# Kernel tuning notes

Measured on AMD Instinct MI355X. Metric: run time of the kernel, lower is better.

Reference implementation:

```python
import jax, jax.numpy as jnp
import numpy as np

N = 50000      # nodes
E = 800000     # edges (avg degree 16)
G = 128        # g_dim (input feature dim)
H1 = 128       # h1_dim (RGCN output dim)
H2 = 32        # h2_dim (per-head channels)
HEADS = 4
R = 6          # num_relations
OUT = H2 * HEADS  # 128, BatchNorm width
BN_EPS = 1e-5


def setup_inputs() -> dict:
    key = jax.random.key(0)
    k = jax.random.split(key, 16)
    s = 0.05
    return {
        "node_features": jax.random.normal(k[0], (N, G), jnp.float32),
        "node_type": jax.random.randint(k[1], (N,), 0, 3),
        "edge_index": jax.random.randint(k[2], (2, E), 0, N),
        "edge_type": jax.random.randint(k[3], (E,), 0, R),
        # RGCNConv params (root_weight=True, bias=True, aggr='mean')
        "W_rel": jax.random.normal(k[4], (R, G, H1), jnp.float32) * s,
        "W_root": jax.random.normal(k[5], (G, H1), jnp.float32) * s,
        "b_rgcn": jnp.zeros((H1,), jnp.float32),
        # TransformerConv params (concat=True, root_weight=True via lin_skip)
        "Wq": jax.random.normal(k[6], (H1, OUT), jnp.float32) * s,
        "bq": jnp.zeros((OUT,), jnp.float32),
        "Wk": jax.random.normal(k[7], (H1, OUT), jnp.float32) * s,
        "bk": jnp.zeros((OUT,), jnp.float32),
        "Wv": jax.random.normal(k[8], (H1, OUT), jnp.float32) * s,
        "bv": jnp.zeros((OUT,), jnp.float32),
        "Wskip": jax.random.normal(k[9], (H1, OUT), jnp.float32) * s,
        "bskip": jnp.zeros((OUT,), jnp.float32),
        # BatchNorm1d affine params
        "bn_gamma": jnp.ones((OUT,), jnp.float32),
        "bn_beta": jnp.zeros((OUT,), jnp.float32),
    }


def _gnn_forward(node_features, edge_index, edge_type,
                 W_rel, W_root, b_rgcn,
                 Wq, bq, Wk, bk, Wv, bv, Wskip, bskip,
                 bn_gamma, bn_beta):
    src, dst = edge_index[0], edge_index[1]  # message flows src (j) -> dst (i)

    # ---- RGCNConv with mean aggregation per relation ----
    # Transform all nodes under every relation: [R, N, H1]
    xt = jnp.einsum('nd,rdo->rno', node_features, W_rel)
    msg = xt[edge_type, src]                          # [E, H1]
    seg = edge_type * N + dst                         # composite (relation, dst) segment id
    agg = jax.ops.segment_sum(msg, seg, num_segments=R * N).reshape(R, N, H1)
    cnt = jax.ops.segment_sum(jnp.ones((E,), msg.dtype), seg,
                              num_segments=R * N).reshape(R, N)
    x = node_features @ W_root + b_rgcn + (agg / jnp.maximum(cnt, 1.0)[:, :, None]).sum(0)

    # ---- TransformerConv (heads=HEADS, concat=True) ----
    q = (x @ Wq + bq).reshape(N, HEADS, H2)
    kk = (x @ Wk + bk).reshape(N, HEADS, H2)
    v = (x @ Wv + bv).reshape(N, HEADS, H2)

    score = (q[dst] * kk[src]).sum(-1) / np.sqrt(H2)  # [E, HEADS]
    m = jax.ops.segment_max(score, dst, num_segments=N)   # -inf for isolated nodes
    m = jnp.where(jnp.isfinite(m), m, 0.0)
    ex = jnp.exp(score - m[dst])
    den = jax.ops.segment_sum(ex, dst, num_segments=N)
    alpha = ex / (den[dst] + 1e-16)                   # [E, HEADS]

    out = jax.ops.segment_sum(alpha[:, :, None] * v[src], dst,
                              num_segments=N).reshape(N, OUT)
    out = out + x @ Wskip + bskip                     # skip / root connection

    # ---- BatchNorm1d (training-mode batch stats) + LeakyReLU(0.01) ----
    mu = out.mean(0)
    var = out.var(0)  # biased, as torch uses for normalization
    y = (out - mu) * jax.lax.rsqrt(var + BN_EPS) * bn_gamma + bn_beta
    return jax.nn.leaky_relu(y, negative_slope=0.01)


def reference(node_features, node_type, edge_index, edge_type,
              W_rel, W_root, b_rgcn,
              Wq, bq, Wk, bk, Wv, bv, Wskip, bskip,
              bn_gamma, bn_beta):
    # node_type is accepted but unused, matching the original forward.
    return _gnn_forward(node_features, edge_index, edge_type,
                        W_rel, W_root, b_rgcn,
                        Wq, bq, Wk, bk, Wv, bv, Wskip, bskip,
                        bn_gamma, bn_beta)
```

## Files before the change

### kernel.cpp

```cpp
#include <hip/hip_runtime.h>
#include <hip/hip_fp16.h>
#include <stdint.h>

#define G      128
#define OUTW   128
#define RNUM   6

typedef unsigned short us;
typedef _Float16 f16x8 __attribute__((ext_vector_type(8)));
typedef float    f32x4 __attribute__((ext_vector_type(4)));

__device__ inline float h2f(us u) { __half h; *(us*)&h = u; return __half2float(h); }
__device__ inline us f2h(float f) { __half h = __float2half(f); return *(us*)&h; }
__device__ inline float2 h22(int u) { return __half22float2(*(__half2*)&u); }

union FragU { f16x8 v; ushort4 u[2]; };

__global__ void count_kernel(const int* __restrict__ ei, const int* __restrict__ et,
                             int* __restrict__ segcnt, int N, int E) {
    int e = blockIdx.x * blockDim.x + threadIdx.x;
    if (e >= E) return;
    int dst = ei[E + e];
    int r   = et[e];
    atomicAdd(&segcnt[dst * RNUM + r], 1);
}

__global__ __launch_bounds__(256)
void scan_part(const int* __restrict__ cnt, int* __restrict__ bsum, int n) {
    __shared__ int s[256];
    int base = blockIdx.x * 1024, t = threadIdx.x;
    int v = 0;
    for (int j = 0; j < 4; ++j) { int idx = base + j * 256 + t; if (idx < n) v += cnt[idx]; }
    s[t] = v; __syncthreads();
    for (int off = 128; off; off >>= 1) { if (t < off) s[t] += s[t + off]; __syncthreads(); }
    if (!t) bsum[blockIdx.x] = s[0];
}

__global__ __launch_bounds__(512)
void scan_top(const int* __restrict__ bsum, int* __restrict__ boff,
              int* __restrict__ segptr, int nb, int n) {
    __shared__ int s[512];
    int t = threadIdx.x;
    int v = (t < nb) ? bsum[t] : 0;
    s[t] = v;
    __syncthreads();
    for (int off = 1; off < 512; off <<= 1) {
        int y = (t >= off) ? s[t - off] : 0;
        __syncthreads();
        s[t] += y;
        __syncthreads();
    }
    if (t < nb) boff[t + 1] = s[t];
    if (!t) boff[0] = 0;
    if (t == nb - 1) segptr[n] = s[t];
}

__global__ __launch_bounds__(256)
void scan_apply(const int* __restrict__ cnt, const int* __restrict__ boff,
                int* __restrict__ segptr, int* __restrict__ cursor, int n) {
    __shared__ int L[1024];
    __shared__ int SS[256];
    int base = blockIdx.x * 1024, t = threadIdx.x;
    for (int j = 0; j < 4; ++j) { int idx = base + j * 256 + t; L[j * 256 + t] = (idx < n) ? cnt[idx] : 0; }
    __syncthreads();
    int s0 = L[t*4] + L[t*4+1] + L[t*4+2] + L[t*4+3];
    SS[t] = s0; __syncthreads();
    for (int off = 1; off < 256; off <<= 1) {
        int y = (t >= off) ? SS[t - off] : 0;
        __syncthreads();
        SS[t] += y;
        __syncthreads();
    }
    int e0 = (t ? SS[t - 1] : 0) + boff[blockIdx.x];
    int4 ov;
    int a;
    a = L[t*4+0]; ov.x = e0; e0 += a;
    a = L[t*4+1]; ov.y = e0; e0 += a;
    a = L[t*4+2]; ov.z = e0; e0 += a;
    a = L[t*4+3]; ov.w = e0; e0 += a;
    int idx0 = base + t * 4;
    if (idx0 + 3 < n) {
        *(int4*)(segptr + idx0) = ov;
        *(int4*)(cursor + idx0) = ov;
    } else {
        int vals[4] = {ov.x, ov.y, ov.z, ov.w};
        for (int k = 0; k < 4; ++k)
            if (idx0 + k < n) { segptr[idx0 + k] = vals[k]; cursor[idx0 + k] = vals[k]; }
    }
}

__global__ void scatter_kernel(const int* __restrict__ ei, const int* __restrict__ et,
                               int* __restrict__ cursor, unsigned* __restrict__ esrc,
                               int N, int E) {
    int e = blockIdx.x * blockDim.x + threadIdx.x;
    if (e >= E) return;
    int src = ei[e];
    int dst = ei[E + e];
    int r   = et[e];
    int pos = atomicAdd(&cursor[dst * RNUM + r], 1);
    esrc[pos] = (unsigned)src;
}

__global__ __launch_bounds__(256)
void prep_kernel(const float* __restrict__ x, us* __restrict__ xh,
                 const float* __restrict__ Wrel, const float* __restrict__ Wroot,
                 ushort4* __restrict__ Btr,
                 const float* __restrict__ Wq, const float* __restrict__ Wk,
                 const float* __restrict__ Wv, const float* __restrict__ Ws,
                 ushort4* __restrict__ Btq, int xblocks) {
    int b = blockIdx.x;
    if (b < xblocks) {
        int i = b * 256 + threadIdx.x;
        float4 a = ((const float4*)x)[2*i];
        float4 c = ((const float4*)x)[2*i+1];
        ushort4 u0 = { f2h(a.x), f2h(a.y), f2h(a.z), f2h(a.w) };
        ushort4 u1 = { f2h(c.x), f2h(c.y), f2h(c.z), f2h(c.w) };
        ((ushort4*)xh)[2*i]   = u0;
        ((ushort4*)xh)[2*i+1] = u1;
    } else if (b < xblocks + 112) {
        int idx = (b - xblocks) * 256 + threadIdx.x;
        int kq = idx >> 7, n = idx & 127;
        ushort4 o;
        us* op = (us*)&o;
#pragma unroll
        for (int i = 0; i < 4; ++i) {
            int k = 4 * kq + i;
            float v = (k < 768) ? Wrel[(size_t)k * 128 + n] : Wroot[(size_t)(k - 768) * 128 + n];
            op[i] = f2h(v);
        }
        Btr[idx] = o;
    } else {
        int idx = (b - xblocks - 112) * 256 + threadIdx.x;
        int kq = idx >> 9, n = idx & 511;
        int quad = n >> 7, nl = n & 127;
        const float* W = (quad == 0) ? Wq : (quad == 1) ? Wk : (quad == 2) ? Wv : Ws;
        ushort4 o;
        us* op = (us*)&o;
#pragma unroll
        for (int i = 0; i < 4; ++i) {
            int k = 4 * kq + i;
            op[i] = f2h(W[(size_t)k * 128 + nl]);
        }
        Btq[idx] = o;
    }
}

__global__ __launch_bounds__(256)
void agg_kernel(const us* __restrict__ xh, const int* __restrict__ segptr,
                const unsigned* __restrict__ esrc, us* __restrict__ meanh, int N) {
    const int wv = threadIdx.x >> 6, l = threadIdx.x & 63;
    const int i = blockIdx.x * 4 + wv;
    if (i >= N) return;
    const int e0 = __builtin_amdgcn_readfirstlane(segptr[i * RNUM]);
    const int e1 = __builtin_amdgcn_readfirstlane(segptr[i * RNUM + RNUM]);

    int rcur = 0;
    int sstart = e0;
    int bnext = __builtin_amdgcn_readfirstlane(segptr[i * RNUM + 1]);
    float2 a = {0.f, 0.f};
    us* wbase = meanh + (size_t)i * 768 + 2 * l;

#define FLUSH() { \
    float sc_ = 1.f / fmaxf((float)(bnext - sstart), 1.f); \
    ushort2 t2_ = { f2h(a.x * sc_), f2h(a.y * sc_) }; \
    *(ushort2*)(wbase + rcur * 128) = t2_; \
    a.x = 0.f; a.y = 0.f; \
    sstart = bnext; ++rcur; \
    if (rcur < RNUM) bnext = __builtin_amdgcn_readfirstlane(segptr[i * RNUM + rcur + 1]); }

#define GET(J) ((unsigned)__shfl((int)pv, (J)))
#define LX(Q)  (*(const ushort2*)(xh + (size_t)(Q) * G + 2 * l))
#define STEP(U) { while (p >= bnext && rcur < RNUM - 1) FLUSH(); \
                  a.x += h2f((U).x); a.y += h2f((U).y); ++p; }

    int p = e0;
    for (int wb = e0; wb < e1; wb += 64) {
        const int nc = min(64, e1 - wb);
        unsigned pv = (wb + l < e1) ? esrc[wb + l] : 0u;
        int j = 0;
        while (j + 8 <= nc) {
            unsigned q0 = GET(j+0), q1 = GET(j+1), q2 = GET(j+2), q3 = GET(j+3);
            unsigned q4 = GET(j+4), q5 = GET(j+5), q6 = GET(j+6), q7 = GET(j+7);
            ushort2 u0 = LX(q0), u1 = LX(q1), u2 = LX(q2), u3 = LX(q3);
            ushort2 u4 = LX(q4), u5 = LX(q5), u6 = LX(q6), u7 = LX(q7);
            STEP(u0); STEP(u1); STEP(u2); STEP(u3);
            STEP(u4); STEP(u5); STEP(u6); STEP(u7);
            j += 8;
        }
        while (j + 2 <= nc) {
            unsigned q0 = GET(j), q1 = GET(j+1);
            ushort2 u0 = LX(q0), u1 = LX(q1);
            STEP(u0); STEP(u1);
            j += 2;
        }
        if (j < nc) {
            unsigned q0 = GET(j);
            ushort2 u0 = LX(q0);
            STEP(u0);
            ++j;
        }
    }
    while (rcur < RNUM) FLUSH();
#undef STEP
#undef LX
#undef GET
#undef FLUSH
}

__global__ __launch_bounds__(256)
void rgcn_mfma4(const us* __restrict__ xh, const us* __restrict__ meanh,
                const ushort4* __restrict__ Btr, const float* __restrict__ brg,
                us* __restrict__ xrh, int N) {
    const int tid = threadIdx.x;
    const int w = tid >> 6, l = tid & 63;
    const int lh = l >> 4, lm = l & 15;
    const int rowbase = blockIdx.x * 128 + w * 32;

    const us* am[2];
    const us* ar[2];
#pragma unroll
    for (int tt = 0; tt < 2; ++tt) {
        int gr = min(rowbase + tt * 16 + lm, N - 1);
        am[tt] = meanh + (size_t)gr * 768;
        ar[tt] = xh + (size_t)gr * 128;
    }

    f32x4 acc[2][8];
#pragma unroll
    for (int tt = 0; tt < 2; ++tt)
#pragma unroll
        for (int ct = 0; ct < 8; ++ct) {
            float b = brg[ct * 16 + lm];
            acc[tt][ct] = (f32x4){b, b, b, b};
        }

    for (int s = 0; s < 24; ++s) {
        const int kqg = s * 8 + lh;
        const ushort4* B0 = Btr + (size_t)kqg * 128 + lm;
        const ushort4* B1 = B0 + 4 * 128;
        FragU bf[8];
#pragma unroll
        for (int ct = 0; ct < 8; ++ct) { bf[ct].u[0] = B0[ct * 16]; bf[ct].u[1] = B1[ct * 16]; }
#pragma unroll
        for (int tt = 0; tt < 2; ++tt) {
            FragU af;
            af.u[0] = *(const ushort4*)(am[tt] + s * 32 + 4 * lh);
            af.u[1] = *(const ushort4*)(am[tt] + s * 32 + 4 * lh + 16);
#pragma unroll
            for (int ct = 0; ct < 8; ++ct)
                acc[tt][ct] = __builtin_amdgcn_mfma_f32_16x16x32_f16(af.v, bf[ct].v, acc[tt][ct], 0, 0, 0);
        }
    }
#pragma unroll
    for (int s = 0; s < 4; ++s) {
        const int kqg = 192 + s * 8 + lh;
        const ushort4* B0 = Btr + (size_t)kqg * 128 + lm;
        const ushort4* B1 = B0 + 4 * 128;
        FragU bf[8];
#pragma unroll
        for (int ct = 0; ct < 8; ++ct) { bf[ct].u[0] = B0[ct * 16]; bf[ct].u[1] = B1[ct * 16]; }
#pragma unroll
        for (int tt = 0; tt < 2; ++tt) {
            FragU af;
            af.u[0] = *(const ushort4*)(ar[tt] + s * 32 + 4 * lh);
            af.u[1] = *(const ushort4*)(ar[tt] + s * 32 + 4 * lh + 16);
#pragma unroll
            for (int ct = 0; ct < 8; ++ct)
                acc[tt][ct] = __builtin_amdgcn_mfma_f32_16x16x32_f16(af.v, bf[ct].v, acc[tt][ct], 0, 0, 0);
        }
    }

#pragma unroll
    for (int tt = 0; tt < 2; ++tt)
#pragma unroll
        for (int ct = 0; ct < 8; ++ct)
#pragma unroll
            for (int i = 0; i < 4; ++i) {
                int r = rowbase + tt * 16 + 4 * lh + i;
                if (r < N) xrh[(size_t)r * 128 + ct * 16 + lm] = f2h(acc[tt][ct][i]);
            }
}

__global__ __launch_bounds__(256)
void qkvs_mfma3(const us* __restrict__ xrh, const ushort4* __restrict__ Btq,
                const float* __restrict__ bq, const float* __restrict__ bk,
                const float* __restrict__ bv, const float* __restrict__ bs,
                us* __restrict__ qsh, us* __restrict__ kvh, int N) {
    const int tid = threadIdx.x;
    const int quad = tid >> 6, l = tid & 63;
    const int lh = l >> 4, lm = l & 15;
    const int base = blockIdx.x * 32;
    const float* bias = (quad == 0) ? bq : (quad == 1) ? bk : (quad == 2) ? bv : bs;

    const us* ap[2];
#pragma unroll
    for (int tt = 0; tt < 2; ++tt) {
        int ar = min(base + tt * 16 + lm, N - 1);
        ap[tt] = xrh + (size_t)ar * 128;
    }

    f32x4 acc[2][8];
#pragma unroll
    for (int tt = 0; tt < 2; ++tt)
#pragma unroll
        for (int ct = 0; ct < 8; ++ct) {
            float b = bias[ct * 16 + lm];
            acc[tt][ct] = (f32x4){b, b, b, b};
        }

#pragma unroll
    for (int s = 0; s < 4; ++s) {
        const int kq = s * 8 + lh;
        const ushort4* B0 = Btq + (size_t)kq * 512 + quad * 128 + lm;
        const ushort4* B1 = B0 + 4 * 512;
        FragU bf[8];
#pragma unroll
        for (int ct = 0; ct < 8; ++ct) { bf[ct].u[0] = B0[ct * 16]; bf[ct].u[1] = B1[ct * 16]; }
#pragma unroll
        for (int tt = 0; tt < 2; ++tt) {
            FragU af;
            af.u[0] = *(const ushort4*)(ap[tt] + kq * 4);
            af.u[1] = *(const ushort4*)(ap[tt] + kq * 4 + 16);
#pragma unroll
            for (int ct = 0; ct < 8; ++ct)
                acc[tt][ct] = __builtin_amdgcn_mfma_f32_16x16x32_f16(af.v, bf[ct].v, acc[tt][ct], 0, 0, 0);
        }
    }

    if (quad == 0 || quad == 3) {
        const int off = (quad == 0) ? 0 : 128;
#pragma unroll
        for (int tt = 0; tt < 2; ++tt)
#pragma unroll
            for (int ct = 0; ct < 8; ++ct)
#pragma unroll
                for (int i = 0; i < 4; ++i) {
                    int r = base + tt * 16 + 4 * lh + i;
                    if (r < N) qsh[(size_t)r * 256 + off + ct * 16 + lm] = f2h(acc[tt][ct][i]);
                }
    } else {
        const int off = (quad == 1) ? 0 : 2;
#pragma unroll
        for (int tt = 0; tt < 2; ++tt)
#pragma unroll
            for (int ct = 0; ct < 8; ++ct)
#pragma unroll
                for (int i = 0; i < 4; ++i) {
                    int r = base + tt * 16 + 4 * lh + i;
                    int col = ct * 16 + lm;
                    if (r < N) kvh[(size_t)r * 256 + (col >> 1) * 4 + (col & 1) + off] = f2h(acc[tt][ct][i]);
                }
    }
}

__global__ __launch_bounds__(256)
void attn_kernel(const us* __restrict__ qsh, const us* __restrict__ kvh,
                 const int* __restrict__ segptr, const unsigned* __restrict__ esrc,
                 float* __restrict__ out, float* __restrict__ bnS,
                 float* __restrict__ bnQ, int N) {
    __shared__ float sS[128], sQ[128];
    const int tid = threadIdx.x;
    if (tid < 128) { sS[tid] = 0.f; sQ[tid] = 0.f; }
    __syncthreads();

    const int wv = tid >> 6, l = tid & 63;
    const int hh = l >> 5, ll = l & 31;
    const int stride = gridDim.x * 8;
    const float QS = 0.17677669529663687f;
    float4 bsum = {0,0,0,0}, bsq = {0,0,0,0};

#define SCORE(D, S) { \
    float2 ka_ = h22((D).x), kb_ = h22((D).z); \
    float t_ = q4.x*ka_.x + q4.y*ka_.y + q4.z*kb_.x + q4.w*kb_.y; \
    t_ += __shfl_xor(t_, 1, 8); t_ += __shfl_xor(t_, 2, 8); t_ += __shfl_xor(t_, 4, 8); \
    S = t_; }

    for (int ibase = blockIdx.x * 8 + wv * 2; ibase < N; ibase += stride) {
        const bool act = (ibase + hh) < N;
        const int i = min(ibase + hh, N - 1);

        int2 qu = *(const int2*)(qsh + (size_t)i * 256 + 4 * ll);
        float2 qa = h22(qu.x), qb = h22(qu.y);
        float4 q4 = { qa.x * QS, qa.y * QS, qb.x * QS, qb.y * QS };

        float m = -INFINITY, den = 0.f;
        float4 acc = {0,0,0,0};
        const int e0 = segptr[(size_t)i * RNUM], e1 = segptr[(size_t)i * RNUM + RNUM];

        for (int wb = e0; wb < e1; wb += 32) {
            const int nc = min(32, e1 - wb);
            unsigned pv = (wb + ll < e1) ? esrc[wb + ll] : 0u;
            int j = 0;
            for (; j + 8 <= nc; j += 8) {
                unsigned p0 = (unsigned)__shfl((int)pv, j+0, 32);
                unsigned p1 = (unsigned)__shfl((int)pv, j+1, 32);
                unsigned p2 = (unsigned)__shfl((int)pv, j+2, 32);
                unsigned p3 = (unsigned)__shfl((int)pv, j+3, 32);
                unsigned p4 = (unsigned)__shfl((int)pv, j+4, 32);
                unsigned p5 = (unsigned)__shfl((int)pv, j+5, 32);
                unsigned p6 = (unsigned)__shfl((int)pv, j+6, 32);
                unsigned p7 = (unsigned)__shfl((int)pv, j+7, 32);
                int4 d0 = *(const int4*)(kvh + (size_t)p0 * 256 + 8 * ll);
                int4 d1 = *(const int4*)(kvh + (size_t)p1 * 256 + 8 * ll);
                int4 d2 = *(const int4*)(kvh + (size_t)p2 * 256 + 8 * ll);
                int4 d3 = *(const int4*)(kvh + (size_t)p3 * 256 + 8 * ll);
                int4 d4 = *(const int4*)(kvh + (size_t)p4 * 256 + 8 * ll);
                int4 d5 = *(const int4*)(kvh + (size_t)p5 * 256 + 8 * ll);
                int4 d6 = *(const int4*)(kvh + (size_t)p6 * 256 + 8 * ll);
                int4 d7 = *(const int4*)(kvh + (size_t)p7 * 256 + 8 * ll);
                float s0, s1, s2, s3, s4, s5, s6, s7;
                SCORE(d0, s0); SCORE(d1, s1); SCORE(d2, s2); SCORE(d3, s3);
                SCORE(d4, s4); SCORE(d5, s5); SCORE(d6, s6); SCORE(d7, s7);
                float mx = fmaxf(m, fmaxf(
                    fmaxf(fmaxf(s0, s1), fmaxf(s2, s3)),
                    fmaxf(fmaxf(s4, s5), fmaxf(s6, s7))));
                float rs = __expf(m - mx);
                float w0 = __expf(s0 - mx), w1 = __expf(s1 - mx);
                float w2 = __expf(s2 - mx), w3 = __expf(s3 - mx);
                float w4 = __expf(s4 - mx), w5 = __expf(s5 - mx);
                float w6 = __expf(s6 - mx), w7 = __expf(s7 - mx);
                den = den * rs + (((w0 + w1) + (w2 + w3)) + ((w4 + w5) + (w6 + w7)));
                float2 va0 = h22(d0.y), vb0 = h22(d0.w);
                float2 va1 = h22(d1.y), vb1 = h22(d1.w);
                float2 va2 = h22(d2.y), vb2 = h22(d2.w);
                float2 va3 = h22(d3.y), vb3 = h22(d3.w);
                float2 va4 = h22(d4.y), vb4 = h22(d4.w);
                float2 va5 = h22(d5.y), vb5 = h22(d5.w);
                float2 va6 = h22(d6.y), vb6 = h22(d6.w);
                float2 va7 = h22(d7.y), vb7 = h22(d7.w);
                acc.x = acc.x * rs + ((w0*va0.x + w1*va1.x) + (w2*va2.x + w3*va3.x))
                                   + ((w4*va4.x + w5*va5.x) + (w6*va6.x + w7*va7.x));
                acc.y = acc.y * rs + ((w0*va0.y + w1*va1.y) + (w2*va2.y + w3*va3.y))
                                   + ((w4*va4.y + w5*va5.y) + (w6*va6.y + w7*va7.y));
                acc.z = acc.z * rs + ((w0*vb0.x + w1*vb1.x) + (w2*vb2.x + w3*vb3.x))
                                   + ((w4*vb4.x + w5*vb5.x) + (w6*vb6.x + w7*vb7.x));
                acc.w = acc.w * rs + ((w0*vb0.y + w1*vb1.y) + (w2*vb2.y + w3*vb3.y))
                                   + ((w4*vb4.y + w5*vb5.y) + (w6*vb6.y + w7*vb7.y));
                m = mx;
            }
            for (; j + 4 <= nc; j += 4) {
                unsigned p0 = (unsigned)__shfl((int)pv, j+0, 32);
                unsigned p1 = (unsigned)__shfl((int)pv, j+1, 32);
                unsigned p2 = (unsigned)__shfl((int)pv, j+2, 32);
                unsigned p3 = (unsigned)__shfl((int)pv, j+3, 32);
                int4 d0 = *(const int4*)(kvh + (size_t)p0 * 256 + 8 * ll);
                int4 d1 = *(const int4*)(kvh + (size_t)p1 * 256 + 8 * ll);
                int4 d2 = *(const int4*)(kvh + (size_t)p2 * 256 + 8 * ll);
                int4 d3 = *(const int4*)(kvh + (size_t)p3 * 256 + 8 * ll);
                float s0, s1, s2, s3;
                SCORE(d0, s0); SCORE(d1, s1); SCORE(d2, s2); SCORE(d3, s3);
                float mx = fmaxf(m, fmaxf(fmaxf(s0, s1), fmaxf(s2, s3)));
                float rs = __expf(m - mx);
                float w0 = __expf(s0 - mx), w1 = __expf(s1 - mx);
                float w2 = __expf(s2 - mx), w3 = __expf(s3 - mx);
                den = den * rs + ((w0 + w1) + (w2 + w3));
                float2 va0 = h22(d0.y), vb0 = h22(d0.w);
                float2 va1 = h22(d1.y), vb1 = h22(d1.w);
                float2 va2 = h22(d2.y), vb2 = h22(d2.w);
                float2 va3 = h22(d3.y), vb3 = h22(d3.w);
                acc.x = acc.x * rs + w0*va0.x + w1*va1.x + w2*va2.x + w3*va3.x;
                acc.y = acc.y * rs + w0*va0.y + w1*va1.y + w2*va2.y + w3*va3.y;
                acc.z = acc.z * rs + w0*vb0.x + w1*vb1.x + w2*vb2.x + w3*vb3.x;
                acc.w = acc.w * rs + w0*vb0.y + w1*vb1.y + w2*vb2.y + w3*vb3.y;
                m = mx;
            }
            for (; j < nc; ++j) {
                unsigned p0 = (unsigned)__shfl((int)pv, j, 32);
                int4 d0 = *(const int4*)(kvh + (size_t)p0 * 256 + 8 * ll);
                float s0; SCORE(d0, s0);
                float mx = fmaxf(m, s0);
                float rs = __expf(m - mx);
                float w0 = __expf(s0 - mx);
                den = den * rs + w0;
                float2 va0 = h22(d0.y), vb0 = h22(d0.w);
                acc.x = acc.x * rs + w0 * va0.x;
                acc.y = acc.y * rs + w0 * va0.y;
                acc.z = acc.z * rs + w0 * vb0.x;
                acc.w = acc.w * rs + w0 * vb0.y;
                m = mx;
            }
        }

        float inv = 1.f / (den + 1e-16f);
        int2 su = *(const int2*)(qsh + (size_t)i * 256 + 128 + 4 * ll);
        float2 sa = h22(su.x), sb = h22(su.y);
        float4 o = { acc.x * inv + sa.x, acc.y * inv + sa.y,
                     acc.z * inv + sb.x, acc.w * inv + sb.y };
        if (act) {
            *(float4*)(out + (size_t)i * OUTW + 4 * ll) = o;
            bsum.x += o.x; bsum.y += o.y; bsum.z += o.z; bsum.w += o.w;
            bsq.x += o.x*o.x; bsq.y += o.y*o.y; bsq.z += o.z*o.z; bsq.w += o.w*o.w;
        }
    }
#undef SCORE

    atomicAdd(&sS[4*ll + 0], bsum.x);
    atomicAdd(&sS[4*ll + 1], bsum.y);
    atomicAdd(&sS[4*ll + 2], bsum.z);
    atomicAdd(&sS[4*ll + 3], bsum.w);
    atomicAdd(&sQ[4*ll + 0], bsq.x);
    atomicAdd(&sQ[4*ll + 1], bsq.y);
    atomicAdd(&sQ[4*ll + 2], bsq.z);
    atomicAdd(&sQ[4*ll + 3], bsq.w);
    __syncthreads();
    if (tid < 128) {
        atomicAdd(&bnS[tid], sS[tid]);
        atomicAdd(&bnQ[tid], sQ[tid]);
    }
}

__global__ __launch_bounds__(256)
void apply_kernel(float* __restrict__ out, const float* __restrict__ bnS,
                  const float* __restrict__ bnQ, const float* __restrict__ gamma,
                  const float* __restrict__ beta, int N, int total4) {
    __shared__ float A_s[128], B_s[128];
    const int tid = threadIdx.x;
    if (tid < 128) {
        float fN  = (float)N;
        float mu  = bnS[tid] / fN;
        float var = bnQ[tid] / fN - mu * mu;
        float rv  = rsqrtf(var + 1e-5f);
        float A   = rv * gamma[tid];
        A_s[tid] = A;
        B_s[tid] = beta[tid] - mu * A;
    }
    __syncthreads();
    for (int idx4 = blockIdx.x * 256 + tid; idx4 < total4; idx4 += gridDim.x * 256) {
        float4 v = ((const float4*)out)[idx4];
        int c0 = (idx4 * 4) & 127;
        float y;
        y = A_s[c0    ] * v.x + B_s[c0    ]; v.x = (y > 0.f) ? y : 0.01f * y;
        y = A_s[c0 + 1] * v.y + B_s[c0 + 1]; v.y = (y > 0.f) ? y : 0.01f * y;
        y = A_s[c0 + 2] * v.z + B_s[c0 + 2]; v.z = (y > 0.f) ? y : 0.01f * y;
        y = A_s[c0 + 3] * v.w + B_s[c0 + 3]; v.w = (y > 0.f) ? y : 0.01f * y;
        ((float4*)out)[idx4] = v;
    }
}

static inline char* alignp(char* p) {
    return (char*)(((uintptr_t)p + 255) & ~(uintptr_t)255);
}

extern "C" void kernel_launch(void* const* d_in, const int* in_sizes, int n_in,
                              void* d_out, int out_size, void* d_ws, size_t ws_size,
                              hipStream_t stream) {
    const float* x     = (const float*)d_in[0];
    const int*   ei    = (const int*)  d_in[2];
    const int*   et    = (const int*)  d_in[3];
    const float* Wrel  = (const float*)d_in[4];
    const float* Wroot = (const float*)d_in[5];
    const float* brg   = (const float*)d_in[6];
    const float* Wq    = (const float*)d_in[7];
    const float* bq    = (const float*)d_in[8];
    const float* Wk    = (const float*)d_in[9];
    const float* bk    = (const float*)d_in[10];
    const float* Wv    = (const float*)d_in[11];
    const float* bv    = (const float*)d_in[12];
    const float* Wsk   = (const float*)d_in[13];
    const float* bsk   = (const float*)d_in[14];
    const float* gamma = (const float*)d_in[15];
    const float* beta  = (const float*)d_in[16];
    float* out = (float*)d_out;

    const int N = in_sizes[0] / G;
    const int E = in_sizes[3];
    const int NSEG = N * RNUM;
    const int NB_SCAN = (NSEG + 1023) / 1024;

    char* w = (char*)d_ws;
    int* segcnt = (int*)w;           w += (size_t)NSEG * 4;
    float* bnS = (float*)w;          w += 128 * 4;
    float* bnQ = (float*)w;          w += 128 * 4;
    size_t zero_bytes = (size_t)(w - (char*)d_ws);
    w = alignp(w);
    int* bsum  = (int*)w;            w += 512 * 4;
    int* boff  = (int*)w;            w += 513 * 4;
    w = alignp(w);
    int* segptr = (int*)w;           w += (size_t)(NSEG + 1) * 4;
    w = alignp(w);
    int* cursor = (int*)w;           w += (size_t)NSEG * 4;
    w = alignp(w);
    unsigned* esrc = (unsigned*)w;   w += (size_t)E * 4;
    w = alignp(w);
    us* xh     = (us*)w;             w += (size_t)N * G * 2;
    w = alignp(w);
    us* xrh    = (us*)w;             w += (size_t)N * OUTW * 2;
    w = alignp(w);
    ushort4* Btr = (ushort4*)w;      w += (size_t)224 * 128 * 8;
    w = alignp(w);
    ushort4* Btq = (ushort4*)w;      w += (size_t)32 * 512 * 8;
    w = alignp(w);
    us* meanh = (us*)w;
    us* qsh   = (us*)w;
    us* kvh   = (us*)(w + (size_t)N * 256 * 2);

    hipMemsetAsync(d_ws, 0, zero_bytes, stream);

    int eb = (E + 255) / 256;
    count_kernel<<<eb, 256, 0, stream>>>(ei, et, segcnt, N, E);

    scan_part<<<NB_SCAN, 256, 0, stream>>>(segcnt, bsum, NSEG);
    scan_top<<<1, 512, 0, stream>>>(bsum, boff, segptr, NB_SCAN, NSEG);
    scan_apply<<<NB_SCAN, 256, 0, stream>>>(segcnt, boff, segptr, cursor, NSEG);

    scatter_kernel<<<eb, 256, 0, stream>>>(ei, et, cursor, esrc, N, E);

    int xblocks = N * G / 8 / 256;
    prep_kernel<<<xblocks + 112 + 64, 256, 0, stream>>>(x, xh, Wrel, Wroot, Btr,
                                                        Wq, Wk, Wv, Wsk, Btq, xblocks);

    agg_kernel<<<(N + 3) / 4, 256, 0, stream>>>(xh, segptr, esrc, meanh, N);

    rgcn_mfma4<<<(N + 127) / 128, 256, 0, stream>>>(xh, meanh, Btr, brg, xrh, N);

    qkvs_mfma3<<<(N + 31) / 32, 256, 0, stream>>>(xrh, Btq, bq, bk, bv, bsk, qsh, kvh, N);

    attn_kernel<<<2048, 256, 0, stream>>>(qsh, kvh, segptr, esrc, out, bnS, bnQ, N);

    int total4 = N * OUTW / 4;
    apply_kernel<<<2048, 256, 0, stream>>>(out, bnS, bnQ, gamma, beta, N, total4);
}
```

Before: 436.9 us.

## Fuse RGCN and QKV/skip GEMMs via LDS; merge count into prep kernel

Fuses the RGCN GEMM with the Q/K/V/skip projection GEMM. The RGCN output tile now stays in shared memory instead of making a round trip through a global fp16 buffer. The edge-count atomics are folded into the prep kernel so one launch disappears, and attention switches from a fixed 2048-block grid to one block per 8 nodes. The trade-off is a smaller QKV grid: 391 blocks instead of 1563, each running four sequential sub-tiles, which may lower parallelism and occupancy.

New measurement: 512.1 us. 1.17x slower.

```diff
diff --git a/kernel.cpp b/kernel.cpp
--- a/kernel.cpp
+++ b/kernel.cpp
@@ -15,15 +15,6 @@
 __device__ inline float2 h22(int u) { return __half22float2(*(__half2*)&u); }
 
 union FragU { f16x8 v; ushort4 u[2]; };
-
-__global__ void count_kernel(const int* __restrict__ ei, const int* __restrict__ et,
-                             int* __restrict__ segcnt, int N, int E) {
-    int e = blockIdx.x * blockDim.x + threadIdx.x;
-    if (e >= E) return;
-    int dst = ei[E + e];
-    int r   = et[e];
-    atomicAdd(&segcnt[dst * RNUM + r], 1);
-}
 
 __global__ __launch_bounds__(256)
 void scan_part(const int* __restrict__ cnt, int* __restrict__ bsum, int n) {
@@ -102,23 +93,32 @@
 }
 
 __global__ __launch_bounds__(256)
-void prep_kernel(const float* __restrict__ x, us* __restrict__ xh,
-                 const float* __restrict__ Wrel, const float* __restrict__ Wroot,
-                 ushort4* __restrict__ Btr,
-                 const float* __restrict__ Wq, const float* __restrict__ Wk,
-                 const float* __restrict__ Wv, const float* __restrict__ Ws,
-                 ushort4* __restrict__ Btq, int xblocks) {
+void prep2_kernel(const int* __restrict__ ei, const int* __restrict__ et,
+                  int* __restrict__ segcnt, int E, int eb,
+                  const float* __restrict__ x, us* __restrict__ xh,
+                  const float* __restrict__ Wrel, const float* __restrict__ Wroot,
+                  ushort4* __restrict__ Btr,
+                  const float* __restrict__ Wq, const float* __restrict__ Wk,
+                  const float* __restrict__ Wv, const float* __restrict__ Ws,
+                  ushort4* __restrict__ Btq, int xblocks) {
     int b = blockIdx.x;
-    if (b < xblocks) {
-        int i = b * 256 + threadIdx.x;
+    if (b < eb) {
+        int e = b * 256 + threadIdx.x;
+        if (e < E) {
+            int dst = ei[E + e];
+            int r   = et[e];
+            atomicAdd(&segcnt[dst * RNUM + r], 1);
+        }
+    } else if (b < eb + xblocks) {
+        int i = (b - eb) * 256 + threadIdx.x;
         float4 a = ((const float4*)x)[2*i];
         float4 c = ((const float4*)x)[2*i+1];
         ushort4 u0 = { f2h(a.x), f2h(a.y), f2h(a.z), f2h(a.w) };
         ushort4 u1 = { f2h(c.x), f2h(c.y), f2h(c.z), f2h(c.w) };
         ((ushort4*)xh)[2*i]   = u0;
         ((ushort4*)xh)[2*i+1] = u1;
-    } else if (b < xblocks + 112) {
-        int idx = (b - xblocks) * 256 + threadIdx.x;
+    } else if (b < eb + xblocks + 112) {
+        int idx = (b - eb - xblocks) * 256 + threadIdx.x;
         int kq = idx >> 7, n = idx & 127;
         ushort4 o;
         us* op = (us*)&o;
@@ -130,7 +130,7 @@
         }
         Btr[idx] = o;
     } else {
-        int idx = (b - xblocks - 112) * 256 + threadIdx.x;
+        int idx = (b - eb - xblocks - 112) * 256 + threadIdx.x;
         int kq = idx >> 9, n = idx & 511;
         int quad = n >> 7, nl = n & 127;
         const float* W = (quad == 0) ? Wq : (quad == 1) ? Wk : (quad == 2) ? Wv : Ws;
@@ -208,148 +208,139 @@
 }
 
 __global__ __launch_bounds__(256)
-void rgcn_mfma4(const us* __restrict__ xh, const us* __restrict__ meanh,
-                const ushort4* __restrict__ Btr, const float* __restrict__ brg,
-                us* __restrict__ xrh, int N) {
+void rgcn_qkvs(const us* __restrict__ xh, const us* __restrict__ meanh,
+               const ushort4* __restrict__ Btr, const float* __restrict__ brg,
+               const ushort4* __restrict__ Btq,
+               const float* __restrict__ bq, const float* __restrict__ bk,
+               const float* __restrict__ bv, const float* __restrict__ bs,
+               us* __restrict__ qsh, us* __restrict__ kvh, int N) {
+    __shared__ us X[128][136];
     const int tid = threadIdx.x;
     const int w = tid >> 6, l = tid & 63;
     const int lh = l >> 4, lm = l & 15;
-    const int rowbase = blockIdx.x * 128 + w * 32;
-
-    const us* am[2];
-    const us* ar[2];
-#pragma unroll
-    for (int tt = 0; tt < 2; ++tt) {
-        int gr = min(rowbase + tt * 16 + lm, N - 1);
-        am[tt] = meanh + (size_t)gr * 768;
-        ar[tt] = xh + (size_t)gr * 128;
-    }
-
-    f32x4 acc[2][8];
-#pragma unroll
-    for (int tt = 0; tt < 2; ++tt)
-#pragma unroll
-        for (int ct = 0; ct < 8; ++ct) {
-            float b = brg[ct * 16 + lm];
-            acc[tt][ct] = (f32x4){b, b, b, b};
-        }
-
-    for (int s = 0; s < 24; ++s) {
-        const int kqg = s * 8 + lh;
-        const ushort4* B0 = Btr + (size_t)kqg * 128 + lm;
-        const ushort4* B1 = B0 + 4 * 128;
-        FragU bf[8];
-#pragma unroll
-        for (int ct = 0; ct < 8; ++ct) { bf[ct].u[0] = B0[ct * 16]; bf[ct].u[1] = B1[ct * 16]; }
+    const int blockbase = blockIdx.x * 128;
+    const int rowbase = blockbase + w * 32;
+
+    {
+        const us* am[2];
+        const us* ar[2];
 #pragma unroll
         for (int tt = 0; tt < 2; ++tt) {
-            FragU af;
-            af.u[0] = *(const ushort4*)(am[tt] + s * 32 + 4 * lh);
-            af.u[1] = *(const ushort4*)(am[tt] + s * 32 + 4 * lh + 16);
+            int gr = min(rowbase + tt * 16 + lm, N - 1);
+            am[tt] = meanh + (size_t)gr * 768;
+            ar[tt] = xh + (size_t)gr * 128;
+        }
+
+        f32x4 acc[2][8];
+#pragma unroll
+        for (int tt = 0; tt < 2; ++tt)
+#pragma unroll
+            for (int ct = 0; ct < 8; ++ct) {
+                float b = brg[ct * 16 + lm];
+                acc[tt][ct] = (f32x4){b, b, b, b};
+            }
+
+        for (int s = 0; s < 24; ++s) {
+            const int kqg = s * 8 + lh;
+            const ushort4* B0 = Btr + (size_t)kqg * 128 + lm;
+            const ushort4* B1 = B0 + 4 * 128;
+            FragU bf[8];
+#pragma unroll
+            for (int ct = 0; ct < 8; ++ct) { bf[ct].u[0] = B0[ct * 16]; bf[ct].u[1] = B1[ct * 16]; }
+#pragma unroll
+            for (int tt = 0; tt < 2; ++tt) {
+                FragU af;
+                af.u[0] = *(const ushort4*)(am[tt] + s * 32 + 4 * lh);
+                af.u[1] = *(const ushort4*)(am[tt] + s * 32 + 4 * lh + 16);
+#pragma unroll
+                for (int ct = 0; ct < 8; ++ct)
+                    acc[tt][ct] = __builtin_amdgcn_mfma_f32_16x16x32_f16(af.v, bf[ct].v, acc[tt][ct], 0, 0, 0);
+            }
+        }
+#pragma unroll
+        for (int s = 0; s < 4; ++s) {
+            const int kqg = 192 + s * 8 + lh;
+            const ushort4* B0 = Btr + (size_t)kqg * 128 + lm;
+            const ushort4* B1 = B0 + 4 * 128;
+            FragU bf[8];
+#pragma unroll
+            for (int ct = 0; ct < 8; ++ct) { bf[ct].u[0] = B0[ct * 16]; bf[ct].u[1] = B1[ct * 16]; }
+#pragma unroll
+            for (int tt = 0; tt < 2; ++tt) {
+                FragU af;
+                af.u[0] = *(const ushort4*)(ar[tt] + s * 32 + 4 * lh);
+                af.u[1] = *(const ushort4*)(ar[tt] + s * 32 + 4 * lh + 16);
+#pragma unroll
+                for (int ct = 0; ct < 8; ++ct)
+                    acc[tt][ct] = __builtin_amdgcn_mfma_f32_16x16x32_f16(af.v, bf[ct].v, acc[tt][ct], 0, 0, 0);
+            }
+        }
+
+#pragma unroll
+        for (int tt = 0; tt < 2; ++tt)
 #pragma unroll
             for (int ct = 0; ct < 8; ++ct)
-                acc[tt][ct] = __builtin_amdgcn_mfma_f32_16x16x32_f16(af.v, bf[ct].v, acc[tt][ct], 0, 0, 0);
-        }
-    }
-#pragma unroll
-    for (int s = 0; s < 4; ++s) {
-        const int kqg = 192 + s * 8 + lh;
-        const ushort4* B0 = Btr + (size_t)kqg * 128 + lm;
-        const ushort4* B1 = B0 + 4 * 128;
-        FragU bf[8];
-#pragma unroll
-        for (int ct = 0; ct < 8; ++ct) { bf[ct].u[0] = B0[ct * 16]; bf[ct].u[1] = B1[ct * 16]; }
-#pragma unroll
-        for (int tt = 0; tt < 2; ++tt) {
-            FragU af;
-            af.u[0] = *(const ushort4*)(ar[tt] + s * 32 + 4 * lh);
-            af.u[1] = *(const ushort4*)(ar[tt] + s * 32 + 4 * lh + 16);
-#pragma unroll
-            for (int ct = 0; ct < 8; ++ct)
-                acc[tt][ct] = __builtin_amdgcn_mfma_f32_16x16x32_f16(af.v, bf[ct].v, acc[tt][ct], 0, 0, 0);
-        }
-    }
-
-#pragma unroll
-    for (int tt = 0; tt < 2; ++tt)
-#pragma unroll
-        for (int ct = 0; ct < 8; ++ct)
-#pragma unroll
-            for (int i = 0; i < 4; ++i) {
-                int r = rowbase + tt * 16 + 4 * lh + i;
-                if (r < N) xrh[(size_t)r * 128 + ct * 16 + lm] = f2h(acc[tt][ct][i]);
-            }
-}
-
-__global__ __launch_bounds__(256)
-void qkvs_mfma3(const us* __restrict__ xrh, const ushort4* __restrict__ Btq,
-                const float* __restrict__ bq, const float* __restrict__ bk,
-                const float* __restrict__ bv, const float* __restrict__ bs,
-                us* __restrict__ qsh, us* __restrict__ kvh, int N) {
-    const int tid = threadIdx.x;
-    const int quad = tid >> 6, l = tid & 63;
-    const int lh = l >> 4, lm = l & 15;
-    const int base = blockIdx.x * 32;
+#pragma unroll
+                for (int i = 0; i < 4; ++i)
+                    X[w * 32 + tt * 16 + 4 * lh + i][ct * 16 + lm] = f2h(acc[tt][ct][i]);
+    }
+    __syncthreads();
+
+    const int quad = w;
     const float* bias = (quad == 0) ? bq : (quad == 1) ? bk : (quad == 2) ? bv : bs;
 
-    const us* ap[2];
-#pragma unroll
-    for (int tt = 0; tt < 2; ++tt) {
-        int ar = min(base + tt * 16 + lm, N - 1);
-        ap[tt] = xrh + (size_t)ar * 128;
-    }
-
-    f32x4 acc[2][8];
-#pragma unroll
-    for (int tt = 0; tt < 2; ++tt)
-#pragma unroll
-        for (int ct = 0; ct < 8; ++ct) {
-            float b = bias[ct * 16 + lm];
-            acc[tt][ct] = (f32x4){b, b, b, b};
-        }
-
-#pragma unroll
-    for (int s = 0; s < 4; ++s) {
-        const int kq = s * 8 + lh;
-        const ushort4* B0 = Btq + (size_t)kq * 512 + quad * 128 + lm;
-        const ushort4* B1 = B0 + 4 * 512;
-        FragU bf[8];
-#pragma unroll
-        for (int ct = 0; ct < 8; ++ct) { bf[ct].u[0] = B0[ct * 16]; bf[ct].u[1] = B1[ct * 16]; }
-#pragma unroll
-        for (int tt = 0; tt < 2; ++tt) {
-            FragU af;
-            af.u[0] = *(const ushort4*)(ap[tt] + kq * 4);
-            af.u[1] = *(const ushort4*)(ap[tt] + kq * 4 + 16);
-#pragma unroll
-            for (int ct = 0; ct < 8; ++ct)
-                acc[tt][ct] = __builtin_amdgcn_mfma_f32_16x16x32_f16(af.v, bf[ct].v, acc[tt][ct], 0, 0, 0);
-        }
-    }
-
-    if (quad == 0 || quad == 3) {
-        const int off = (quad == 0) ? 0 : 128;
+    for (int tp = 0; tp < 4; ++tp) {
+        f32x4 a2[2][8];
 #pragma unroll
         for (int tt = 0; tt < 2; ++tt)
 #pragma unroll
-            for (int ct = 0; ct < 8; ++ct)
-#pragma unroll
-                for (int i = 0; i < 4; ++i) {
-                    int r = base + tt * 16 + 4 * lh + i;
-                    if (r < N) qsh[(size_t)r * 256 + off + ct * 16 + lm] = f2h(acc[tt][ct][i]);
-                }
-    } else {
-        const int off = (quad == 1) ? 0 : 2;
-#pragma unroll
-        for (int tt = 0; tt < 2; ++tt)
-#pragma unroll
-            for (int ct = 0; ct < 8; ++ct)
-#pragma unroll
-                for (int i = 0; i < 4; ++i) {
-                    int r = base + tt * 16 + 4 * lh + i;
-                    int col = ct * 16 + lm;
-                    if (r < N) kvh[(size_t)r * 256 + (col >> 1) * 4 + (col & 1) + off] = f2h(acc[tt][ct][i]);
-                }
+            for (int ct = 0; ct < 8; ++ct) {
+                float b = bias[ct * 16 + lm];
+                a2[tt][ct] = (f32x4){b, b, b, b};
+            }
+#pragma unroll
+        for (int s = 0; s < 4; ++s) {
+            const int kq = s * 8 + lh;
+            const ushort4* B0 = Btq + (size_t)kq * 512 + quad * 128 + lm;
+            const ushort4* B1 = B0 + 4 * 512;
+            FragU bf[8];
+#pragma unroll
+            for (int ct = 0; ct < 8; ++ct) { bf[ct].u[0] = B0[ct * 16]; bf[ct].u[1] = B1[ct * 16]; }
+#pragma unroll
+            for (int tt = 0; tt < 2; ++tt) {
+                const int row = tp * 32 + tt * 16 + lm;
+                FragU af;
+                af.u[0] = *(const ushort4*)(&X[row][4 * kq]);
+                af.u[1] = *(const ushort4*)(&X[row][4 * kq + 16]);
+#pragma unroll
+                for (int ct = 0; ct < 8; ++ct)
+                    a2[tt][ct] = __builtin_amdgcn_mfma_f32_16x16x32_f16(af.v, bf[ct].v, a2[tt][ct], 0, 0, 0);
+            }
+        }
+        if (quad == 0 || quad == 3) {
+            const int off = (quad == 0) ? 0 : 128;
+#pragma unroll
+            for (int tt = 0; tt < 2; ++tt)
+#pragma unroll
+                for (int ct = 0; ct < 8; ++ct)
+#pragma unroll
+                    for (int i = 0; i < 4; ++i) {
+                        int r = blockbase + tp * 32 + tt * 16 + 4 * lh + i;
+                        if (r < N) qsh[(size_t)r * 256 + off + ct * 16 + lm] = f2h(a2[tt][ct][i]);
+                    }
+        } else {
+            const int off = (quad == 1) ? 0 : 2;
+#pragma unroll
+            for (int tt = 0; tt < 2; ++tt)
+#pragma unroll
+                for (int ct = 0; ct < 8; ++ct)
+#pragma unroll
+                    for (int i = 0; i < 4; ++i) {
+                        int r = blockbase + tp * 32 + tt * 16 + 4 * lh + i;
+                        int col = ct * 16 + lm;
+                        if (r < N) kvh[(size_t)r * 256 + (col >> 1) * 4 + (col & 1) + off] = f2h(a2[tt][ct][i]);
+                    }
+        }
     }
 }
 
@@ -584,8 +575,6 @@
     w = alignp(w);
     us* xh     = (us*)w;             w += (size_t)N * G * 2;
     w = alignp(w);
-    us* xrh    = (us*)w;             w += (size_t)N * OUTW * 2;
-    w = alignp(w);
     ushort4* Btr = (ushort4*)w;      w += (size_t)224 * 128 * 8;
     w = alignp(w);
     ushort4* Btq = (ushort4*)w;      w += (size_t)32 * 512 * 8;
@@ -597,7 +586,9 @@
     hipMemsetAsync(d_ws, 0, zero_bytes, stream);
 
     int eb = (E + 255) / 256;
-    count_kernel<<<eb, 256, 0, stream>>>(ei, et, segcnt, N, E);
+    int xblocks = N * G / 8 / 256;
+    prep2_kernel<<<eb + xblocks + 112 + 64, 256, 0, stream>>>(
+        ei, et, segcnt, E, eb, x, xh, Wrel, Wroot, Btr, Wq, Wk, Wv, Wsk, Btq, xblocks);
 
     scan_part<<<NB_SCAN, 256, 0, stream>>>(segcnt, bsum, NSEG);
     scan_top<<<1, 512, 0, stream>>>(bsum, boff, segptr, NB_SCAN, NSEG);
@@ -605,17 +596,12 @@
 
     scatter_kernel<<<eb, 256, 0, stream>>>(ei, et, cursor, esrc, N, E);
 
-    int xblocks = N * G / 8 / 256;
-    prep_kernel<<<xblocks + 112 + 64, 256, 0, stream>>>(x, xh, Wrel, Wroot, Btr,
-                                                        Wq, Wk, Wv, Wsk, Btq, xblocks);
-
     agg_kernel<<<(N + 3) / 4, 256, 0, stream>>>(xh, segptr, esrc, meanh, N);
 
-    rgcn_mfma4<<<(N + 127) / 128, 256, 0, stream>>>(xh, meanh, Btr, brg, xrh, N);
-
-    qkvs_mfma3<<<(N + 31) / 32, 256, 0, stream>>>(xrh, Btq, bq, bk, bv, bsk, qsh, kvh, N);
-
-    attn_kernel<<<2048, 256, 0, stream>>>(qsh, kvh, segptr, esrc, out, bnS, bnQ, N);
+    rgcn_qkvs<<<(N + 127) / 128, 256, 0, stream>>>(xh, meanh, Btr, brg, Btq,
+                                                   bq, bk, bv, bsk, qsh, kvh, N);
+
+    attn_kernel<<<(N + 7) / 8, 256, 0, stream>>>(qsh, kvh, segptr, esrc, out, bnS, bnQ, N);
 
     int total4 = N * OUTW / 4;
     apply_kernel<<<2048, 256, 0, stream>>>(out, bnS, bnQ, gamma, beta, N, total4);
```
